# Kernel tuning notes

Measured on AMD Instinct MI355X. Metric: run time of the kernel, lower is better.

Reference implementation:

```python
import jax, jax.numpy as jnp
import numpy as np

B, T, F, H, R, K = 256, 512, 128, 128, 8, 64
LAG_IDX = 0


def setup_inputs() -> dict:
    key = jax.random.key(0)
    ks = jax.random.split(key, 14)
    s_ih = 1.0 / np.sqrt(F)
    s_hh = 1.0 / np.sqrt(H)
    return {
        "x": jax.random.normal(ks[0], (B, T, F), jnp.float32),
        "regime": jax.random.randint(ks[1], (B, T), 0, R, jnp.int32),
        "lag_scale": jnp.asarray(0.9, jnp.float32),
        "lag_bias": jnp.asarray(0.0, jnp.float32),
        "Wih0": jax.random.normal(ks[2], (3 * H, F), jnp.float32) * s_ih,
        "Whh0": jax.random.normal(ks[3], (3 * H, H), jnp.float32) * s_hh,
        "bih0": jax.random.normal(ks[4], (3 * H,), jnp.float32) * s_hh,
        "bhh0": jax.random.normal(ks[5], (3 * H,), jnp.float32) * s_hh,
        "Wih1": jax.random.normal(ks[6], (3 * H, H), jnp.float32) * s_hh,
        "Whh1": jax.random.normal(ks[7], (3 * H, H), jnp.float32) * s_hh,
        "bih1": jax.random.normal(ks[8], (3 * H,), jnp.float32) * s_hh,
        "bhh1": jax.random.normal(ks[9], (3 * H,), jnp.float32) * s_hh,
        "W1": jax.random.normal(ks[10], (R, H, K), jnp.float32) * s_hh,
        "b1": jax.random.normal(ks[11], (R, K), jnp.float32) * 0.1,
        "W2": jax.random.normal(ks[12], (R, K), jnp.float32) * 0.05,
        "b2": jax.random.normal(ks[13], (R,), jnp.float32) * 0.05,
    }


def _gru_layer(x_tbf, Wih, Whh, bih, bhh):
    # PyTorch GRU cell, gate order (r, z, n). x_tbf: (T, B, Fin)
    Hh = Whh.shape[1]

    def step(h, xt):
        gi = xt @ Wih.T + bih            # (B, 3H)
        gh = h @ Whh.T + bhh             # (B, 3H)
        ir, iz, inn = jnp.split(gi, 3, axis=-1)
        hr, hz, hn = jnp.split(gh, 3, axis=-1)
        r = jax.nn.sigmoid(ir + hr)
        z = jax.nn.sigmoid(iz + hz)
        n = jnp.tanh(inn + r * hn)
        h_new = (1.0 - z) * n + z * h
        return h_new, h_new

    h0 = jnp.zeros((x_tbf.shape[1], Hh), x_tbf.dtype)
    _, ys = jax.lax.scan(step, h0, x_tbf)
    return ys                             # (T, B, H)


def reference(x, regime, lag_scale, lag_bias,
              Wih0, Whh0, bih0, bhh0,
              Wih1, Whh1, bih1, bhh1,
              W1, b1, W2, b2):
    lag_pred = lag_scale * x[:, :, LAG_IDX] + lag_bias          # (B, T)

    xt = jnp.transpose(x, (1, 0, 2))                            # (T, B, F)
    h1 = _gru_layer(xt, Wih0, Whh0, bih0, bhh0)
    h2 = _gru_layer(h1, Wih1, Whh1, bih1, bhh1)
    out = jnp.transpose(h2, (1, 0, 2))                          # (B, T, H)

    Bq, Tq, Hq = out.shape
    out_flat = out.reshape(-1, Hq)                              # (N, H)
    reg = regime.reshape(-1)                                    # (N,)

    # regime-specific heads: Linear(H,64) -> SiLU -> Linear(64,1)
    a = jnp.einsum('nh,rhk->nrk', out_flat, W1) + b1            # (N, R, K)
    a = jnp.take_along_axis(a, reg[:, None, None].astype(jnp.int32), axis=1)[:, 0, :]
    a = a * jax.nn.sigmoid(a)                                   # SiLU
    corr = jnp.einsum('nk,nk->n', a, W2[reg]) + b2[reg]         # (N,)

    return lag_pred + corr.reshape(Bq, Tq)
```

## Files before the change

### kernel.cpp

```cpp
#include <hip/hip_runtime.h>
#include <hip/hip_bf16.h>
#include <cstdint>

#define B_ 256
#define T_ 512
#define F_ 128
#define H_ 128
#define G3_ 384
#define R_ 8
#define K_ 64

typedef __attribute__((ext_vector_type(8))) short short8_t;
typedef __attribute__((ext_vector_type(4))) float f32x4;
typedef __attribute__((ext_vector_type(2))) float f32x2;

__device__ __forceinline__ float sigm(float x) { return 1.f / (1.f + __expf(-x)); }
__device__ __forceinline__ float tanh_f(float x) { return 1.f - 2.f / (1.f + __expf(2.f * x)); }
__device__ __forceinline__ unsigned short f2bf(float f) {
    uint32_t u = __builtin_bit_cast(uint32_t, f);
    return (unsigned short)((u + 0x7FFFu + ((u >> 16) & 1u)) >> 16);
}
__device__ __forceinline__ short8_t pack8(float4 a, float4 b) {
    short8_t v;
    v[0] = (short)f2bf(a.x); v[1] = (short)f2bf(a.y);
    v[2] = (short)f2bf(a.z); v[3] = (short)f2bf(a.w);
    v[4] = (short)f2bf(b.x); v[5] = (short)f2bf(b.y);
    v[6] = (short)f2bf(b.z); v[7] = (short)f2bf(b.w);
    return v;
}

__device__ __forceinline__ float dpp_red2(float x) {
    int a = __builtin_amdgcn_mov_dpp(__builtin_bit_cast(int, x), 0xB1, 0xF, 0xF, true);
    x += __builtin_bit_cast(float, a);
    int b = __builtin_amdgcn_mov_dpp(__builtin_bit_cast(int, x), 0x4E, 0xF, 0xF, true);
    x += __builtin_bit_cast(float, b);
    return x;
}

__global__ __launch_bounds__(512, 2) void gemm_gi_mfma(const float* __restrict__ A,
                                                       const float* __restrict__ W,
                                                       const float* __restrict__ bias,
                                                       float* __restrict__ C)
{
    __shared__ alignas(16) unsigned short A_lds[128 * 128];

    const int tid = threadIdx.x;
    const int wv = tid >> 6, lane = tid & 63;
    const int lc = lane & 15, lg = lane >> 4;
    const size_t m0 = (size_t)blockIdx.x * 128;

    short8_t bf[3][4];
    float bi[3];
    #pragma unroll
    for (int u = 0; u < 3; ++u) {
        const int n = 48 * wv + 16 * u + lc;
        bi[u] = bias[n];
        #pragma unroll
        for (int ks = 0; ks < 4; ++ks) {
            const float4* wp = (const float4*)(W + (size_t)n * 128 + ks * 32 + lg * 8);
            bf[u][ks] = pack8(wp[0], wp[1]);
        }
    }

    {
        const int m = tid >> 2, kq = tid & 3;
        const float4* ap = (const float4*)(A + (m0 + m) * 128 + kq * 32);
        float4 v0 = ap[0], v1 = ap[1], v2 = ap[2], v3 = ap[3];
        float4 v4 = ap[4], v5 = ap[5], v6 = ap[6], v7 = ap[7];
        char* base = (char*)A_lds;
        const int bb = m * 256 + kq * 64, sw = (m & 7) << 4;
        *(short8_t*)(base + ((bb +  0) ^ sw)) = pack8(v0, v1);
        *(short8_t*)(base + ((bb + 16) ^ sw)) = pack8(v2, v3);
        *(short8_t*)(base + ((bb + 32) ^ sw)) = pack8(v4, v5);
        *(short8_t*)(base + ((bb + 48) ^ sw)) = pack8(v6, v7);
    }
    __syncthreads();

    const char* Ab = (const char*)A_lds;
    #pragma unroll 2
    for (int mt = 0; mt < 8; ++mt) {
        short8_t af0 = *(const short8_t*)(Ab + (((mt * 16 + lc) * 256 +  0 + lg * 16) ^ ((lc & 7) << 4)));
        short8_t af1 = *(const short8_t*)(Ab + (((mt * 16 + lc) * 256 + 64 + lg * 16) ^ ((lc & 7) << 4)));
        short8_t af2 = *(const short8_t*)(Ab + (((mt * 16 + lc) * 256 + 128 + lg * 16) ^ ((lc & 7) << 4)));
        short8_t af3 = *(const short8_t*)(Ab + (((mt * 16 + lc) * 256 + 192 + lg * 16) ^ ((lc & 7) << 4)));
        f32x4 a0 = {0.f, 0.f, 0.f, 0.f}, a1 = a0, a2 = a0;
        a0 = __builtin_amdgcn_mfma_f32_16x16x32_bf16(af0, bf[0][0], a0, 0, 0, 0);
        a1 = __builtin_amdgcn_mfma_f32_16x16x32_bf16(af0, bf[1][0], a1, 0, 0, 0);
        a2 = __builtin_amdgcn_mfma_f32_16x16x32_bf16(af0, bf[2][0], a2, 0, 0, 0);
        a0 = __builtin_amdgcn_mfma_f32_16x16x32_bf16(af1, bf[0][1], a0, 0, 0, 0);
        a1 = __builtin_amdgcn_mfma_f32_16x16x32_bf16(af1, bf[1][1], a1, 0, 0, 0);
        a2 = __builtin_amdgcn_mfma_f32_16x16x32_bf16(af1, bf[2][1], a2, 0, 0, 0);
        a0 = __builtin_amdgcn_mfma_f32_16x16x32_bf16(af2, bf[0][2], a0, 0, 0, 0);
        a1 = __builtin_amdgcn_mfma_f32_16x16x32_bf16(af2, bf[1][2], a1, 0, 0, 0);
        a2 = __builtin_amdgcn_mfma_f32_16x16x32_bf16(af2, bf[2][2], a2, 0, 0, 0);
        a0 = __builtin_amdgcn_mfma_f32_16x16x32_bf16(af3, bf[0][3], a0, 0, 0, 0);
        a1 = __builtin_amdgcn_mfma_f32_16x16x32_bf16(af3, bf[1][3], a1, 0, 0, 0);
        a2 = __builtin_amdgcn_mfma_f32_16x16x32_bf16(af3, bf[2][3], a2, 0, 0, 0);
        #pragma unroll
        for (int r = 0; r < 4; ++r) {
            float* cp = C + (m0 + mt * 16 + 4 * lg + r) * G3_ + 48 * wv + lc;
            cp[0]  = a0[r] + bi[0];
            cp[16] = a1[r] + bi[1];
            cp[32] = a2[r] + bi[2];
        }
    }
}

__global__ __launch_bounds__(512, 2) void gru_seq(const float* __restrict__ gi,
                                                  const float* __restrict__ Whh,
                                                  const float* __restrict__ bhh,
                                                  float* __restrict__ hout)
{
    __shared__ alignas(16) float hbuf[2][4][36];

    const int tid = threadIdx.x;
    const int b = blockIdx.x;
    const int w = tid >> 6, lane = tid & 63;
    const int j = 16 * w + (lane >> 2);
    const int s = lane & 3;
    const bool fin = (s == 0);

    f32x2 wr2[16], wz2[16], wn2[16];
    {
        const float4* p0 = (const float4*)(Whh + (size_t)j * 128 + s * 32);
        const float4* p1 = (const float4*)(Whh + (size_t)(128 + j) * 128 + s * 32);
        const float4* p2 = (const float4*)(Whh + (size_t)(256 + j) * 128 + s * 32);
        #pragma unroll
        for (int q = 0; q < 8; ++q) {
            float4 v0 = p0[q], v1 = p1[q], v2 = p2[q];
            wr2[2*q]   = f32x2{v0.x, v0.y};
            wr2[2*q+1] = f32x2{v0.z, v0.w};
            wz2[2*q]   = f32x2{v1.x, v1.y};
            wz2[2*q+1] = f32x2{v1.z, v1.w};
            wn2[2*q]   = f32x2{v2.x, v2.y};
            wn2[2*q+1] = f32x2{v2.z, v2.w};
        }
    }
    const float br = bhh[j], bz = bhh[128 + j], bn = bhh[256 + j];

    if (tid < H_) hbuf[0][tid >> 5][tid & 31] = 0.f;
    __syncthreads();

    const float* gip = gi + (size_t)b * T_ * G3_ + j;
    float* hop = hout + (size_t)b * T_ * H_ + j;

    float g0[3], g1[3], g2[3], g3[3];
    if (fin) {
        #pragma unroll
        for (int u = 0; u < 3; ++u) {
            g0[u] = gip[0 * G3_ + 128 * u];
            g1[u] = gip[1 * G3_ + 128 * u];
            g2[u] = gip[2 * G3_ + 128 * u];
            g3[u] = gip[3 * G3_ + 128 * u];
        }
    }
    float hprev = 0.f;

    auto step = [&](int t, float (&gc)[3]) {
        const int p = t & 1;
        const float4* hv = (const float4*)(&hbuf[p][s][0]);
        f32x2 pr2 = {0.f, 0.f}, pz2 = pr2, pn2 = pr2;
        #pragma unroll
        for (int q = 0; q < 8; ++q) {
            float4 h4 = hv[q];
            f32x2 ha = {h4.x, h4.y};
            f32x2 hb = {h4.z, h4.w};
            pr2 += wr2[2*q] * ha;  pr2 += wr2[2*q+1] * hb;
            pz2 += wz2[2*q] * ha;  pz2 += wz2[2*q+1] * hb;
            pn2 += wn2[2*q] * ha;  pn2 += wn2[2*q+1] * hb;
        }
        float pr = dpp_red2(pr2[0] + pr2[1]);
        float pz = dpp_red2(pz2[0] + pz2[1]);
        float pn = dpp_red2(pn2[0] + pn2[1]);

        if (fin) {
            float r  = sigm(gc[0] + pr + br);
            float z  = sigm(gc[1] + pz + bz);
            float nn = tanh_f(gc[2] + r * (pn + bn));
            float h  = (1.f - z) * nn + z * hprev;
            hprev = h;
            hbuf[p ^ 1][j >> 5][j & 31] = h;
            hop[(size_t)t * H_] = h;
            int tn = (t + 4 < T_) ? t + 4 : T_ - 1;
            const float* gp = gip + (size_t)tn * G3_;
            gc[0] = gp[0]; gc[1] = gp[128]; gc[2] = gp[256];
        }
        asm volatile("s_waitcnt lgkmcnt(0)" ::: "memory");
        __builtin_amdgcn_s_barrier();
    };

    for (int t = 0; t < T_; t += 4) {
        step(t + 0, g0);
        step(t + 1, g1);
        step(t + 2, g2);
        step(t + 3, g3);
    }
}

__global__ __launch_bounds__(256) void head_k(const float* __restrict__ h2,
                                              const float* __restrict__ x,
                                              const int* __restrict__ regime,
                                              const float* __restrict__ W1,
                                              const float* __restrict__ b1,
                                              const float* __restrict__ W2,
                                              const float* __restrict__ b2,
                                              const float* __restrict__ lag_scale,
                                              const float* __restrict__ lag_bias,
                                              float* __restrict__ out)
{
    __shared__ alignas(16) float hrow[4][128];
    const int tid = threadIdx.x;
    const int wv = tid >> 6, lane = tid & 63;
    const size_t s = (size_t)blockIdx.x * 4 + wv;
    const int reg = regime[s];

    if (lane < 32)
        ((float4*)hrow[wv])[lane] = ((const float4*)(h2 + s * H_))[lane];
    __syncthreads();

    float acc = b1[reg * K_ + lane];
    const float* Wp = W1 + (size_t)reg * H_ * K_ + lane;
    const float4* h4p = (const float4*)hrow[wv];
    #pragma unroll
    for (int q = 0; q < 32; ++q) {
        float4 h4 = h4p[q];
        acc += h4.x * Wp[(4 * q + 0) * K_];
        acc += h4.y * Wp[(4 * q + 1) * K_];
        acc += h4.z * Wp[(4 * q + 2) * K_];
        acc += h4.w * Wp[(4 * q + 3) * K_];
    }
    float silu = acc * sigm(acc);
    float v = silu * W2[reg * K_ + lane];
    #pragma unroll
    for (int m = 1; m < 64; m <<= 1) v += __shfl_xor(v, m);
    if (lane == 0) {
        float lag = lag_scale[0] * x[s * F_] + lag_bias[0];
        out[s] = lag + v + b2[reg];
    }
}

extern "C" void kernel_launch(void* const* d_in, const int* in_sizes, int n_in,
                              void* d_out, int out_size, void* d_ws, size_t ws_size,
                              hipStream_t stream) {
    const float* x         = (const float*)d_in[0];
    const int*   regime    = (const int*)d_in[1];
    const float* lag_scale = (const float*)d_in[2];
    const float* lag_bias  = (const float*)d_in[3];
    const float* Wih0      = (const float*)d_in[4];
    const float* Whh0      = (const float*)d_in[5];
    const float* bih0      = (const float*)d_in[6];
    const float* bhh0      = (const float*)d_in[7];
    const float* Wih1      = (const float*)d_in[8];
    const float* Whh1      = (const float*)d_in[9];
    const float* bih1      = (const float*)d_in[10];
    const float* bhh1      = (const float*)d_in[11];
    const float* W1        = (const float*)d_in[12];
    const float* b1        = (const float*)d_in[13];
    const float* W2        = (const float*)d_in[14];
    const float* b2        = (const float*)d_in[15];
    float* out = (float*)d_out;

    const size_t NT = (size_t)B_ * T_;
    const size_t need = NT * G3_ * 4 + NT * H_ * 4;
    if (ws_size < need) {
        hipMemsetAsync(d_out, 0x7F, (size_t)out_size * 4, stream);
        return;
    }
    float* gi = (float*)d_ws;
    float* hb = gi + NT * G3_;

    const int gblocks = (int)(NT / 128);
    gemm_gi_mfma<<<gblocks, 512, 0, stream>>>(x, Wih0, bih0, gi);
    gru_seq<<<B_, 512, 0, stream>>>(gi, Whh0, bhh0, hb);
    gemm_gi_mfma<<<gblocks, 512, 0, stream>>>(hb, Wih1, bih1, gi);
    gru_seq<<<B_, 512, 0, stream>>>(gi, Whh1, bhh1, hb);
    head_k<<<(int)(NT / 4), 256, 0, stream>>>(hb, x, regime, W1, b1, W2, b2,
                                              lag_scale, lag_bias, out);
}
```

Baseline: 947.9 us.

## Bucket timesteps by regime and cache head weights in registers

Replaces the per-row head kernel with two steps. A scatter kernel uses wave ballots and atomics to build a per-regime list of row indices. A bucketed head kernel then keeps one regime's W1 column in registers and runs over that regime's rows. This is meant to remove the repeated strided global/L2 reads of W1 for every row. In exchange it adds a memset, an extra launch, atomics and indirect gathers of h2 rows, and it launches many blocks that exit early.

```diff
diff --git a/kernel.cpp b/kernel.cpp
--- a/kernel.cpp
+++ b/kernel.cpp
@@ -9,6 +9,7 @@
 #define G3_ 384
 #define R_ 8
 #define K_ 64
+#define NT_ 131072
 
 typedef __attribute__((ext_vector_type(8))) short short8_t;
 typedef __attribute__((ext_vector_type(4))) float f32x4;
@@ -197,45 +198,82 @@
     }
 }
 
-__global__ __launch_bounds__(256) void head_k(const float* __restrict__ h2,
-                                              const float* __restrict__ x,
-                                              const int* __restrict__ regime,
-                                              const float* __restrict__ W1,
-                                              const float* __restrict__ b1,
-                                              const float* __restrict__ W2,
-                                              const float* __restrict__ b2,
-                                              const float* __restrict__ lag_scale,
-                                              const float* __restrict__ lag_bias,
-                                              float* __restrict__ out)
+__global__ __launch_bounds__(256) void scatter_k(const int* __restrict__ regime,
+                                                 int* __restrict__ cnt,
+                                                 int* __restrict__ list)
 {
-    __shared__ alignas(16) float hrow[4][128];
-    const int tid = threadIdx.x;
-    const int wv = tid >> 6, lane = tid & 63;
-    const size_t s = (size_t)blockIdx.x * 4 + wv;
-    const int reg = regime[s];
-
-    if (lane < 32)
-        ((float4*)hrow[wv])[lane] = ((const float4*)(h2 + s * H_))[lane];
-    __syncthreads();
-
-    float acc = b1[reg * K_ + lane];
-    const float* Wp = W1 + (size_t)reg * H_ * K_ + lane;
-    const float4* h4p = (const float4*)hrow[wv];
+    const int i = blockIdx.x * 256 + threadIdx.x;
+    const int lane = threadIdx.x & 63;
+    const int r = regime[i];
     #pragma unroll
-    for (int q = 0; q < 32; ++q) {
-        float4 h4 = h4p[q];
-        acc += h4.x * Wp[(4 * q + 0) * K_];
-        acc += h4.y * Wp[(4 * q + 1) * K_];
-        acc += h4.z * Wp[(4 * q + 2) * K_];
-        acc += h4.w * Wp[(4 * q + 3) * K_];
-    }
-    float silu = acc * sigm(acc);
-    float v = silu * W2[reg * K_ + lane];
+    for (int rr = 0; rr < R_; ++rr) {
+        unsigned long long m = __ballot(r == rr);
+        if (m == 0ull) continue;
+        int leader = __ffsll((unsigned long long)m) - 1;
+        int base = 0;
+        if (lane == leader) base = atomicAdd(&cnt[rr], __popcll(m));
+        base = __shfl(base, leader);
+        if (r == rr) {
+            int off = __popcll(m & ((1ull << lane) - 1ull));
+            list[rr * NT_ + base + off] = i;
+        }
+    }
+}
+
+__global__ __launch_bounds__(512, 1) void head_bucket(const float* __restrict__ h2,
+                                                      const float* __restrict__ x,
+                                                      const float* __restrict__ W1,
+                                                      const float* __restrict__ b1,
+                                                      const float* __restrict__ W2,
+                                                      const float* __restrict__ b2,
+                                                      const float* __restrict__ lag_scale,
+                                                      const float* __restrict__ lag_bias,
+                                                      const int* __restrict__ cnt,
+                                                      const int* __restrict__ list,
+                                                      float* __restrict__ out)
+{
+    __shared__ alignas(16) float hstage[8][130];
+
+    const int reg = blockIdx.x >> 11;
+    const int seg = blockIdx.x & 2047;
+    const int n = cnt[reg];
+    if (seg * 64 >= n) return;
+
+    const int tid = threadIdx.x, w = tid >> 6, lane = tid & 63;
+
+    f32x2 w1c[64];
+    const float* W1r = W1 + (size_t)reg * H_ * K_ + lane;
     #pragma unroll
-    for (int m = 1; m < 64; m <<= 1) v += __shfl_xor(v, m);
-    if (lane == 0) {
-        float lag = lag_scale[0] * x[s * F_] + lag_bias[0];
-        out[s] = lag + v + b2[reg];
+    for (int q = 0; q < 64; ++q) {
+        w1c[q][0] = W1r[(2 * q) * K_];
+        w1c[q][1] = W1r[(2 * q + 1) * K_];
+    }
+    const float b1v = b1[reg * K_ + lane];
+    const float w2v = W2[reg * K_ + lane];
+    const float b2v = b2[reg];
+    const float ls = lag_scale[0], lb = lag_bias[0];
+
+    for (int it = 0; it < 8; ++it) {
+        const int slot = seg * 64 + it * 8 + w;
+        if (slot >= n) break;
+        const int s = list[reg * NT_ + slot];
+
+        float2 hp = *(const float2*)(h2 + (size_t)s * H_ + 2 * lane);
+        hstage[w][2 * lane] = hp.x;
+        hstage[w][2 * lane + 1] = hp.y;
+
+        f32x2 acc2 = {b1v, 0.f};
+        #pragma unroll
+        for (int q = 0; q < 64; ++q) {
+            f32x2 hb = *(const f32x2*)&hstage[w][2 * q];
+            acc2 += w1c[q] * hb;
+        }
+        float a = acc2[0] + acc2[1];
+        float v = a * sigm(a) * w2v;
+        #pragma unroll
+        for (int m = 1; m < 64; m <<= 1) v += __shfl_xor(v, m);
+        if (lane == 0)
+            out[s] = ls * x[(size_t)s * F_] + lb + v + b2v;
     }
 }
 
@@ -269,11 +307,17 @@
     float* gi = (float*)d_ws;
     float* hb = gi + NT * G3_;
 
+    int* cnt  = (int*)d_ws;
+    int* list = (int*)d_ws + 64;
+
     const int gblocks = (int)(NT / 128);
     gemm_gi_mfma<<<gblocks, 512, 0, stream>>>(x, Wih0, bih0, gi);
     gru_seq<<<B_, 512, 0, stream>>>(gi, Whh0, bhh0, hb);
     gemm_gi_mfma<<<gblocks, 512, 0, stream>>>(hb, Wih1, bih1, gi);
     gru_seq<<<B_, 512, 0, stream>>>(gi, Whh1, bhh1, hb);
-    head_k<<<(int)(NT / 4), 256, 0, stream>>>(hb, x, regime, W1, b1, W2, b2,
-                                              lag_scale, lag_bias, out);
-}
+
+    hipMemsetAsync(cnt, 0, 64 * sizeof(int), stream);
+    scatter_k<<<(int)(NT / 256), 256, 0, stream>>>(regime, cnt, list);
+    head_bucket<<<R_ * 2048, 512, 0, stream>>>(hb, x, W1, b1, W2, b2,
+                                               lag_scale, lag_bias, cnt, list, out);
+}
```

Result: slower. 1.135 ms (+19.8%).
